# Optimization experiments

Measured on AMD Instinct MI355X. Metric: run time of the kernel, lower is better.

## Reference

```python
import jax, jax.numpy as jnp
import numpy as np

B, HID, FH, O = 8192, 1024, 96, 8
E = O + O * (O - 1) // 2  # 36 eta params per step


def setup_inputs() -> dict:
    key = jax.random.key(0)
    ks = jax.random.split(key, 9)
    w = lambda k, sh: (jax.random.normal(k, sh, jnp.float32) * 0.02)
    return {
        "z": jax.random.normal(ks[0], (B, HID), jnp.float32),
        "W1": w(ks[1], (HID, HID)), "b1": jnp.zeros((HID,), jnp.float32),
        "W2": w(ks[2], (HID, HID)), "b2": jnp.zeros((HID,), jnp.float32),
        "Wm": w(ks[3], (HID, FH * O)), "bm": jnp.zeros((FH * O,), jnp.float32),
        "Wv": w(ks[4], (HID, FH * E)), "bv": jnp.zeros((FH * E,), jnp.float32),
    }


def reference(z, W1, b1, W2, b2, Wm, bm, Wv, bv):
    # FeedForward decoder (expansion_factor=1, dropout inactive at eval)
    h = jax.nn.silu(z @ W1 + b1) @ W2 + b2                     # [B, HID]
    means = (h @ Wm + bm).reshape(B, FH, O)                    # [B, FH, O]
    log_var = (h @ Wv + bv).reshape(B, FH, E)                  # [B, FH, E]
    eta_d = log_var[..., :O]                                   # diagonal params
    eta_T = log_var[..., O:]                                   # strict upper-tri params

    d = jnp.exp(0.5 * eta_d)                                   # [B, FH, O]
    eye = jnp.eye(O, dtype=z.dtype)
    D = d[..., :, None] * eye                                  # diag_embed(d)
    Dinv_T_scale = (1.0 / d)[..., :, None]                     # rows of D^{-1}

    iu = np.triu_indices(O, k=1)
    T = jnp.broadcast_to(eye, (B, FH, O, O)).at[..., iu[0], iu[1]].set(eta_T)

    # precision = T^T @ D^{-1} @ T ; D^{-1} @ T scales rows of T
    precision = jnp.einsum('bhji,bhjk->bhik', T, T * Dinv_T_scale)
    return means, precision, D, T
```

## Files before the change

kernel.cpp:

```cpp
#include <hip/hip_runtime.h>
#include <math.h>

#define BATCH 8192
#define HID   1024
#define FH    96
#define OO    8
#define EE    36
#define NLV   (FH*EE)
#define NM    (FH*OO)

typedef short  bf16x8 __attribute__((ext_vector_type(8)));
typedef float  f32x4  __attribute__((ext_vector_type(4)));
typedef unsigned short u16x8 __attribute__((ext_vector_type(8)));

static const size_t OFF_P = (size_t)BATCH * FH * OO;
static const size_t OFF_D = OFF_P + (size_t)BATCH * FH * 64;
static const size_t OFF_T = OFF_D + (size_t)BATCH * FH * 64;

__device__ __forceinline__ unsigned short f2bf(float f) {
    unsigned int u = __float_as_uint(f);
    u += 0x7fffu + ((u >> 16) & 1u);
    return (unsigned short)(u >> 16);
}
__device__ __forceinline__ float bf2f(unsigned short s) {
    return __uint_as_float(((unsigned int)s) << 16);
}

__device__ __forceinline__ size_t blk_off(int r, int k) {
    return ((size_t)(r >> 7)) * (128 * HID) + (size_t)(k >> 3) * 1024
         + (size_t)(r & 127) * 8 + (size_t)(k & 7);
}

__device__ __forceinline__ void glds16(const unsigned short* g, unsigned short* l) {
    __builtin_amdgcn_global_load_lds(
        (const __attribute__((address_space(1))) unsigned int*)g,
        (__attribute__((address_space(3))) unsigned int*)l, 16, 0, 0);
}

__global__ __launch_bounds__(256) void conv_blockify(const float* __restrict__ X,
                                                     unsigned short* __restrict__ Xh,
                                                     unsigned short* __restrict__ Xl)
{
    int idx  = blockIdx.x * 256 + threadIdx.x;
    int row  = idx & 127;
    int kgrp = (idx >> 7) & 127;
    int rblk = idx >> 14;
    const float* src = X + ((size_t)(rblk * 128 + row)) * HID + kgrp * 8;
    float4 v0 = reinterpret_cast<const float4*>(src)[0];
    float4 v1 = reinterpret_cast<const float4*>(src)[1];
    float vv[8] = {v0.x, v0.y, v0.z, v0.w, v1.x, v1.y, v1.z, v1.w};
    u16x8 h, l;
#pragma unroll
    for (int j = 0; j < 8; ++j) {
        unsigned short hh = f2bf(vv[j]);
        h[j] = hh;
        l[j] = f2bf(vv[j] - bf2f(hh));
    }
    *reinterpret_cast<u16x8*>(Xh + (size_t)idx * 8) = h;
    *reinterpret_cast<u16x8*>(Xl + (size_t)idx * 8) = l;
}

__global__ __launch_bounds__(256) void transpose_split_blk(const float* __restrict__ W,
                                                           unsigned short* __restrict__ Th,
                                                           unsigned short* __restrict__ Tl,
                                                           int N)
{
    __shared__ float sh[32][33];
    const int tx = threadIdx.x;
    const int ty = threadIdx.y;
    const int n0 = blockIdx.x * 32;
    const int k0 = blockIdx.y * 32;
#pragma unroll
    for (int i = 0; i < 4; ++i) {
        int kl = ty + i * 8;
        sh[kl][tx] = W[(size_t)(k0 + kl) * N + n0 + tx];
    }
    __syncthreads();
#pragma unroll
    for (int i = 0; i < 4; ++i) {
        int nl = ty + i * 8;
        float v = sh[tx][nl];
        unsigned short h = f2bf(v);
        unsigned short l = f2bf(v - bf2f(h));
        size_t o = blk_off(n0 + nl, k0 + tx);
        Th[o] = h;
        Tl[o] = l;
    }
}

template<int ACT, int OUTBLK>
__global__ __launch_bounds__(256) void gemm_bs(
    const unsigned short* __restrict__ Ah_, const unsigned short* __restrict__ Al_,
    const unsigned short* __restrict__ Bh_, const unsigned short* __restrict__ Bl_,
    const float* __restrict__ bias,
    float* __restrict__ Cf,
    unsigned short* __restrict__ Ch, unsigned short* __restrict__ Cl,
    int N)
{
    __shared__ unsigned short AhL[4096];
    __shared__ unsigned short AlL[4096];
    __shared__ unsigned short BhL[4096];
    __shared__ unsigned short BlL[4096];

    const int tid  = threadIdx.x;
    const int lane = tid & 63;
    const int wave = tid >> 6;
    const int m0   = blockIdx.x * 128;
    const int n0   = blockIdx.y * 128;
    const int wm0  = (wave >> 1) * 64;
    const int wn0  = (wave & 1) * 64;
    const int l15  = lane & 15;
    const int l4   = lane >> 4;

    const unsigned short* Ah = Ah_ + (size_t)(m0 >> 7) * (128 * HID);
    const unsigned short* Al = Al_ + (size_t)(m0 >> 7) * (128 * HID);
    const unsigned short* Bh = Bh_ + (size_t)(n0 >> 7) * (128 * HID);
    const unsigned short* Bl = Bl_ + (size_t)(n0 >> 7) * (128 * HID);

    f32x4 acc[4][4];
#pragma unroll
    for (int i = 0; i < 4; ++i)
#pragma unroll
        for (int j = 0; j < 4; ++j)
            acc[i][j] = (f32x4){0.f, 0.f, 0.f, 0.f};

    const int c0 = wave * 2;
    const int c1 = c0 + 1;

    for (int k0 = 0; k0 < HID; k0 += 32) {
        __syncthreads();
        const size_t tb = (size_t)(k0 >> 3) * 1024;
        const size_t o0 = tb + (size_t)c0 * 512 + (size_t)lane * 8;
        const size_t o1 = tb + (size_t)c1 * 512 + (size_t)lane * 8;
        glds16(Ah + o0, AhL + c0 * 512);
        glds16(Ah + o1, AhL + c1 * 512);
        glds16(Al + o0, AlL + c0 * 512);
        glds16(Al + o1, AlL + c1 * 512);
        glds16(Bh + o0, BhL + c0 * 512);
        glds16(Bh + o1, BhL + c1 * 512);
        glds16(Bl + o0, BlL + c0 * 512);
        glds16(Bl + o1, BlL + c1 * 512);
        __syncthreads();

        bf16x8 a_h[4], a_l[4];
#pragma unroll
        for (int mf = 0; mf < 4; ++mf) {
            int off = l4 * 1024 + (wm0 + mf * 16 + l15) * 8;
            a_h[mf] = *reinterpret_cast<const bf16x8*>(&AhL[off]);
            a_l[mf] = *reinterpret_cast<const bf16x8*>(&AlL[off]);
        }
#pragma unroll
        for (int nf = 0; nf < 4; ++nf) {
            int off = l4 * 1024 + (wn0 + nf * 16 + l15) * 8;
            bf16x8 b_h = *reinterpret_cast<const bf16x8*>(&BhL[off]);
            bf16x8 b_l = *reinterpret_cast<const bf16x8*>(&BlL[off]);
#pragma unroll
            for (int mf = 0; mf < 4; ++mf) {
                acc[mf][nf] = __builtin_amdgcn_mfma_f32_16x16x32_bf16(a_h[mf], b_h, acc[mf][nf], 0, 0, 0);
                acc[mf][nf] = __builtin_amdgcn_mfma_f32_16x16x32_bf16(a_h[mf], b_l, acc[mf][nf], 0, 0, 0);
                acc[mf][nf] = __builtin_amdgcn_mfma_f32_16x16x32_bf16(a_l[mf], b_h, acc[mf][nf], 0, 0, 0);
            }
        }
    }

#pragma unroll
    for (int nf = 0; nf < 4; ++nf) {
        int gc = n0 + wn0 + nf * 16 + l15;
        float bb = bias[gc];
#pragma unroll
        for (int mf = 0; mf < 4; ++mf) {
#pragma unroll
            for (int r = 0; r < 4; ++r) {
                int gr = m0 + wm0 + mf * 16 + l4 * 4 + r;
                float o = acc[mf][nf][r] + bb;
                if (ACT) o = o / (1.f + __expf(-o));
                if (OUTBLK == 0) {
                    Cf[(size_t)gr * N + gc] = o;
                } else {
                    unsigned short h = f2bf(o);
                    unsigned short l = f2bf(o - bf2f(h));
                    size_t off = blk_off(gr, gc);
                    Ch[off] = h;
                    Cl[off] = l;
                }
            }
        }
    }
}

__global__ __launch_bounds__(256) void mcd_epilogue(const float* __restrict__ lv,
                                                    float* __restrict__ out)
{
    const int gid  = blockIdx.x * 256 + threadIdx.x;
    const int row  = gid / FH;
    const int head = gid - row * FH;

    const float* src = lv + (size_t)row * NLV + head * EE;
    float e[EE];
#pragma unroll
    for (int i = 0; i < 9; ++i)
        *reinterpret_cast<float4*>(&e[i * 4]) =
            reinterpret_cast<const float4*>(src)[i];

    float dv[OO], invd[OO];
#pragma unroll
    for (int i = 0; i < OO; ++i) {
        dv[i]   = __expf(0.5f * e[i]);
        invd[i] = 1.f / dv[i];
    }

    float Tu[OO][OO];
#pragma unroll
    for (int j = 0; j < OO; ++j) {
#pragma unroll
        for (int i = j + 1; i < OO; ++i) {
            Tu[j][i] = e[OO + j * 7 - (j * (j - 1)) / 2 + (i - j - 1)];
        }
    }

    float* Pp = out + OFF_P + (size_t)gid * 64;
    float* Dp = out + OFF_D + (size_t)gid * 64;
    float* Tp = out + OFF_T + (size_t)gid * 64;

#pragma unroll
    for (int i = 0; i < OO; ++i) {
        float rowv[OO];
#pragma unroll
        for (int k = 0; k < OO; ++k) {
            float s = 0.f;
#pragma unroll
            for (int j = 0; j < OO; ++j) {
                if (j <= i && j <= k) {
                    float tji = (j == i) ? 1.f : Tu[j][i];
                    float tjk = (j == k) ? 1.f : Tu[j][k];
                    s = fmaf(tji, tjk * invd[j], s);
                }
            }
            rowv[k] = s;
        }
        *reinterpret_cast<float4*>(Pp + i * 8)     = make_float4(rowv[0], rowv[1], rowv[2], rowv[3]);
        *reinterpret_cast<float4*>(Pp + i * 8 + 4) = make_float4(rowv[4], rowv[5], rowv[6], rowv[7]);
    }

#pragma unroll
    for (int i = 0; i < OO; ++i) {
        float rowv[OO];
#pragma unroll
        for (int k = 0; k < OO; ++k) rowv[k] = (k == i) ? dv[i] : 0.f;
        *reinterpret_cast<float4*>(Dp + i * 8)     = make_float4(rowv[0], rowv[1], rowv[2], rowv[3]);
        *reinterpret_cast<float4*>(Dp + i * 8 + 4) = make_float4(rowv[4], rowv[5], rowv[6], rowv[7]);
    }

#pragma unroll
    for (int j = 0; j < OO; ++j) {
        float rowv[OO];
#pragma unroll
        for (int k = 0; k < OO; ++k)
            rowv[k] = (k < j) ? 0.f : (k == j) ? 1.f : Tu[j][k];
        *reinterpret_cast<float4*>(Tp + j * 8)     = make_float4(rowv[0], rowv[1], rowv[2], rowv[3]);
        *reinterpret_cast<float4*>(Tp + j * 8 + 4) = make_float4(rowv[4], rowv[5], rowv[6], rowv[7]);
    }
}

extern "C" void kernel_launch(void* const* d_in, const int* in_sizes, int n_in,
                              void* d_out, int out_size, void* d_ws, size_t ws_size,
                              hipStream_t stream)
{
    (void)in_sizes; (void)n_in; (void)out_size; (void)ws_size;
    const float* z  = (const float*)d_in[0];
    const float* W1 = (const float*)d_in[1];
    const float* b1 = (const float*)d_in[2];
    const float* W2 = (const float*)d_in[3];
    const float* b2 = (const float*)d_in[4];
    const float* Wm = (const float*)d_in[5];
    const float* bm = (const float*)d_in[6];
    const float* Wv = (const float*)d_in[7];
    const float* bv = (const float*)d_in[8];
    float* out = (float*)d_out;

    const size_t EL = (size_t)BATCH * HID;

    float* lv = (float*)d_ws;
    unsigned short* zh  = (unsigned short*)d_ws;
    unsigned short* zl  = zh  + EL;
    unsigned short* h1h = zl  + EL;
    unsigned short* h1l = h1h + EL;
    unsigned short* hh  = (unsigned short*)(lv + (size_t)BATCH * NLV);
    unsigned short* hl  = hh  + EL;
    unsigned short* W1h = hl  + EL;
    unsigned short* W1l = W1h + (size_t)HID * HID;
    unsigned short* W2h = W1l + (size_t)HID * HID;
    unsigned short* W2l = W2h + (size_t)HID * HID;
    unsigned short* Wmh = W2l + (size_t)HID * HID;
    unsigned short* Wml = Wmh + (size_t)NM * HID;
    unsigned short* Wvh = Wml + (size_t)NM * HID;
    unsigned short* Wvl = Wvh + (size_t)NLV * HID;

    dim3 tb(32, 8);
    conv_blockify<<<dim3(4096), 256, 0, stream>>>(z, zh, zl);
    transpose_split_blk<<<dim3(HID / 32, HID / 32), tb, 0, stream>>>(W1, W1h, W1l, HID);
    transpose_split_blk<<<dim3(HID / 32, HID / 32), tb, 0, stream>>>(W2, W2h, W2l, HID);
    transpose_split_blk<<<dim3(NM  / 32, HID / 32), tb, 0, stream>>>(Wm, Wmh, Wml, NM);
    transpose_split_blk<<<dim3(NLV / 32, HID / 32), tb, 0, stream>>>(Wv, Wvh, Wvl, NLV);

    gemm_bs<1, 1><<<dim3(BATCH / 128, HID / 128), 256, 0, stream>>>(
        zh, zl, W1h, W1l, b1, nullptr, h1h, h1l, HID);
    gemm_bs<0, 1><<<dim3(BATCH / 128, HID / 128), 256, 0, stream>>>(
        h1h, h1l, W2h, W2l, b2, nullptr, hh, hl, HID);
    gemm_bs<0, 0><<<dim3(BATCH / 128, NM / 128), 256, 0, stream>>>(
        hh, hl, Wmh, Wml, bm, out, nullptr, nullptr, NM);
    gemm_bs<0, 0><<<dim3(BATCH / 128, NLV / 128), 256, 0, stream>>>(
        hh, hl, Wvh, Wvl, bv, lv, nullptr, nullptr, NLV);

    mcd_epilogue<<<dim3(BATCH * FH / 256), 256, 0, stream>>>(lv, out);
}
```

Baseline: 1.184 ms.

## Double-buffer GEMM LDS tiles and transpose MFMA operands for vectorized stores

Splits the shared-memory tiles into two buffers so the global-to-LDS load of the next K slice overlaps the MFMA work on the current one, cutting the two barriers per iteration to one. It also swaps the A and B operands in the MFMAs so each lane holds four consecutive output columns. That lets the epilogue use float4 bias loads and float4 or 4-wide bf16 stores in place of scalar ones. It also simplifies the index math in the epilogue kernel. Shared memory use doubles, which may reduce occupancy, and the single barrier depends on async load ordering being correct.

```diff
diff --git a/kernel.cpp b/kernel.cpp
--- a/kernel.cpp
+++ b/kernel.cpp
@@ -12,6 +12,7 @@
 typedef short  bf16x8 __attribute__((ext_vector_type(8)));
 typedef float  f32x4  __attribute__((ext_vector_type(4)));
 typedef unsigned short u16x8 __attribute__((ext_vector_type(8)));
+typedef unsigned short u16x4 __attribute__((ext_vector_type(4)));
 
 static const size_t OFF_P = (size_t)BATCH * FH * OO;
 static const size_t OFF_D = OFF_P + (size_t)BATCH * FH * 64;
@@ -97,10 +98,7 @@
     unsigned short* __restrict__ Ch, unsigned short* __restrict__ Cl,
     int N)
 {
-    __shared__ unsigned short AhL[4096];
-    __shared__ unsigned short AlL[4096];
-    __shared__ unsigned short BhL[4096];
-    __shared__ unsigned short BlL[4096];
+    __shared__ unsigned short L[2][4][4096];
 
     const int tid  = threadIdx.x;
     const int lane = tid & 63;
@@ -127,62 +125,80 @@
     const int c0 = wave * 2;
     const int c1 = c0 + 1;
 
-    for (int k0 = 0; k0 < HID; k0 += 32) {
-        __syncthreads();
+    auto stage = [&](int buf, int k0) {
         const size_t tb = (size_t)(k0 >> 3) * 1024;
         const size_t o0 = tb + (size_t)c0 * 512 + (size_t)lane * 8;
         const size_t o1 = tb + (size_t)c1 * 512 + (size_t)lane * 8;
-        glds16(Ah + o0, AhL + c0 * 512);
-        glds16(Ah + o1, AhL + c1 * 512);
-        glds16(Al + o0, AlL + c0 * 512);
-        glds16(Al + o1, AlL + c1 * 512);
-        glds16(Bh + o0, BhL + c0 * 512);
-        glds16(Bh + o1, BhL + c1 * 512);
-        glds16(Bl + o0, BlL + c0 * 512);
-        glds16(Bl + o1, BlL + c1 * 512);
-        __syncthreads();
+        glds16(Ah + o0, &L[buf][0][c0 * 512]);
+        glds16(Ah + o1, &L[buf][0][c1 * 512]);
+        glds16(Al + o0, &L[buf][1][c0 * 512]);
+        glds16(Al + o1, &L[buf][1][c1 * 512]);
+        glds16(Bh + o0, &L[buf][2][c0 * 512]);
+        glds16(Bh + o1, &L[buf][2][c1 * 512]);
+        glds16(Bl + o0, &L[buf][3][c0 * 512]);
+        glds16(Bl + o1, &L[buf][3][c1 * 512]);
+    };
+
+    stage(0, 0);
+    __syncthreads();
+
+    int buf = 0;
+    for (int k0 = 0; k0 < HID; k0 += 32) {
+        if (k0 + 32 < HID) stage(buf ^ 1, k0 + 32);
 
         bf16x8 a_h[4], a_l[4];
 #pragma unroll
         for (int mf = 0; mf < 4; ++mf) {
             int off = l4 * 1024 + (wm0 + mf * 16 + l15) * 8;
-            a_h[mf] = *reinterpret_cast<const bf16x8*>(&AhL[off]);
-            a_l[mf] = *reinterpret_cast<const bf16x8*>(&AlL[off]);
+            a_h[mf] = *reinterpret_cast<const bf16x8*>(&L[buf][0][off]);
+            a_l[mf] = *reinterpret_cast<const bf16x8*>(&L[buf][1][off]);
         }
 #pragma unroll
         for (int nf = 0; nf < 4; ++nf) {
             int off = l4 * 1024 + (wn0 + nf * 16 + l15) * 8;
-            bf16x8 b_h = *reinterpret_cast<const bf16x8*>(&BhL[off]);
-            bf16x8 b_l = *reinterpret_cast<const bf16x8*>(&BlL[off]);
+            bf16x8 b_h = *reinterpret_cast<const bf16x8*>(&L[buf][2][off]);
+            bf16x8 b_l = *reinterpret_cast<const bf16x8*>(&L[buf][3][off]);
 #pragma unroll
             for (int mf = 0; mf < 4; ++mf) {
-                acc[mf][nf] = __builtin_amdgcn_mfma_f32_16x16x32_bf16(a_h[mf], b_h, acc[mf][nf], 0, 0, 0);
-                acc[mf][nf] = __builtin_amdgcn_mfma_f32_16x16x32_bf16(a_h[mf], b_l, acc[mf][nf], 0, 0, 0);
-                acc[mf][nf] = __builtin_amdgcn_mfma_f32_16x16x32_bf16(a_l[mf], b_h, acc[mf][nf], 0, 0, 0);
+                acc[mf][nf] = __builtin_amdgcn_mfma_f32_16x16x32_bf16(b_h, a_h[mf], acc[mf][nf], 0, 0, 0);
+                acc[mf][nf] = __builtin_amdgcn_mfma_f32_16x16x32_bf16(b_l, a_h[mf], acc[mf][nf], 0, 0, 0);
+                acc[mf][nf] = __builtin_amdgcn_mfma_f32_16x16x32_bf16(b_h, a_l[mf], acc[mf][nf], 0, 0, 0);
             }
         }
-    }
-
-#pragma unroll
-    for (int nf = 0; nf < 4; ++nf) {
-        int gc = n0 + wn0 + nf * 16 + l15;
-        float bb = bias[gc];
-#pragma unroll
-        for (int mf = 0; mf < 4; ++mf) {
-#pragma unroll
-            for (int r = 0; r < 4; ++r) {
-                int gr = m0 + wm0 + mf * 16 + l4 * 4 + r;
-                float o = acc[mf][nf][r] + bb;
-                if (ACT) o = o / (1.f + __expf(-o));
-                if (OUTBLK == 0) {
-                    Cf[(size_t)gr * N + gc] = o;
-                } else {
-                    unsigned short h = f2bf(o);
-                    unsigned short l = f2bf(o - bf2f(h));
-                    size_t off = blk_off(gr, gc);
-                    Ch[off] = h;
-                    Cl[off] = l;
+        __syncthreads();
+        buf ^= 1;
+    }
+
+#pragma unroll
+    for (int mf = 0; mf < 4; ++mf) {
+        int gm = m0 + wm0 + mf * 16 + l15;
+#pragma unroll
+        for (int nf = 0; nf < 4; ++nf) {
+            int nq = wn0 + nf * 16 + l4 * 4;
+            float4 bb = *reinterpret_cast<const float4*>(bias + n0 + nq);
+            float o[4];
+            o[0] = acc[mf][nf][0] + bb.x;
+            o[1] = acc[mf][nf][1] + bb.y;
+            o[2] = acc[mf][nf][2] + bb.z;
+            o[3] = acc[mf][nf][3] + bb.w;
+            if (ACT) {
+#pragma unroll
+                for (int r = 0; r < 4; ++r) o[r] = o[r] / (1.f + __expf(-o[r]));
+            }
+            if (OUTBLK == 0) {
+                *reinterpret_cast<float4*>(Cf + (size_t)gm * N + n0 + nq) =
+                    make_float4(o[0], o[1], o[2], o[3]);
+            } else {
+                u16x4 hv, lv4;
+#pragma unroll
+                for (int r = 0; r < 4; ++r) {
+                    unsigned short hh = f2bf(o[r]);
+                    hv[r] = hh;
+                    lv4[r] = f2bf(o[r] - bf2f(hh));
                 }
+                size_t off = blk_off(gm, n0 + nq);
+                *reinterpret_cast<u16x4*>(Ch + off) = hv;
+                *reinterpret_cast<u16x4*>(Cl + off) = lv4;
             }
         }
     }
@@ -192,10 +208,8 @@
                                                     float* __restrict__ out)
 {
     const int gid  = blockIdx.x * 256 + threadIdx.x;
-    const int row  = gid / FH;
-    const int head = gid - row * FH;
-
-    const float* src = lv + (size_t)row * NLV + head * EE;
+
+    const float* src = lv + (size_t)gid * EE;
     float e[EE];
 #pragma unroll
     for (int i = 0; i < 9; ++i)
```

Result: no change. 1.168 ms (-1.4%).
